# Kernel optimization log

Hardware: AMD Instinct MI355X
Metric: run time of the kernel (lower is better)

Reference implementation:

```python
import jax, jax.numpy as jnp
import numpy as np

B, D, N = 8, 512, 4096
HEADS, DH = 8, 64
HID = HEADS * DH  # 512
SCALE = DH ** -0.5


def setup_inputs() -> dict:
    key = jax.random.key(0)
    k0, k1, k2, k3 = jax.random.split(key, 4)
    x = jax.random.normal(k0, (B, D, N), dtype=jnp.float32)
    w_qkv = jax.random.normal(k1, (3 * HID, D), dtype=jnp.float32) * 0.02
    w_out = jax.random.normal(k2, (D, HID), dtype=jnp.float32) * 0.02
    b_out = jax.random.normal(k3, (D,), dtype=jnp.float32) * 0.02
    g = jnp.ones((1, D, 1), dtype=jnp.float32)
    return {"x": x, "w_qkv": w_qkv, "w_out": w_out, "b_out": b_out, "g": g}


def reference(x, w_qkv, w_out, b_out, g):
    # 1x1 Conv1d (no bias) == channel matmul: [b, 3*HID, n]
    qkv = jnp.einsum('od,bdn->bon', w_qkv, x)
    q, k, v = jnp.split(qkv, 3, axis=1)
    # b (h c) n -> b h c n
    q = q.reshape(B, HEADS, DH, N)
    k = k.reshape(B, HEADS, DH, N)
    v = v.reshape(B, HEADS, DH, N)
    q = jax.nn.softmax(q, axis=2) * SCALE  # softmax over feature dim d
    k = jax.nn.softmax(k, axis=3)          # softmax over sequence dim n
    context = jnp.einsum('bhdn,bhen->bhde', k, v)   # [b,h,d,e]
    out = jnp.einsum('bhde,bhdn->bhen', context, q)  # [b,h,e,n]
    out = out.reshape(B, HID, N)
    # 1x1 Conv1d with bias
    y = jnp.einsum('oh,bhn->bon', w_out, out) + b_out[None, :, None]
    # RMSNorm: F.normalize(y, dim=1) * g * sqrt(D)
    norm = jnp.sqrt(jnp.sum(y * y, axis=1, keepdims=True))
    y = y / jnp.maximum(norm, 1e-12) * g * jnp.asarray(D, y.dtype) ** 0.5
    return y
```

## Files before the change

### kernel.cpp

```cpp
#include <hip/hip_runtime.h>
#include <math.h>

#define B 8
#define D 512
#define N 4096
#define HEADS 8
#define DH 64
#define HID 512
#define O3 1536
#define KDIM 512
#define SCALE 0.125f
#define SQRT_D 22.62741699796952f

typedef __attribute__((ext_vector_type(4))) float f32x4;
typedef __attribute__((ext_vector_type(8))) short bf16x8;

static __device__ __forceinline__ unsigned short f2bf(float f) {
    unsigned int u = __float_as_uint(f);
    unsigned int r = (u + 0x7fffu + ((u >> 16) & 1u)) >> 16;
    return (unsigned short)r;
}

static __device__ __forceinline__ float bf2f(unsigned short u) {
    return __uint_as_float((unsigned int)u << 16);
}

static __device__ __forceinline__ void gload_lds16(const void* g, void* l) {
    __builtin_amdgcn_global_load_lds(
        (const __attribute__((address_space(1))) unsigned int*)g,
        (__attribute__((address_space(3))) unsigned int*)l, 16, 0, 0);
}

__global__ __launch_bounds__(256) void prep(const float* __restrict__ x,
                                            unsigned short* __restrict__ xT,
                                            const float* __restrict__ w,
                                            unsigned short* __restrict__ wb) {
    if (blockIdx.z == B) {
        int i = ((blockIdx.y * 96 + blockIdx.x) * 256 + threadIdx.x) * 4;
        float4 v = *(const float4*)(w + i);
        __align__(8) unsigned short o[4] = {f2bf(v.x), f2bf(v.y), f2bf(v.z), f2bf(v.w)};
        *(uint2*)(wb + i) = *(const uint2*)o;
        return;
    }
    if (blockIdx.x >= 64) return;
    __shared__ float tile[64][65];
    const int n0 = blockIdx.x * 64, d0 = blockIdx.y * 64, b = blockIdx.z;
    const float* xb = x + (size_t)b * D * N;
    unsigned short* xTb = xT + (size_t)b * N * KDIM;
    const int t = threadIdx.x;
    const int r = t >> 4, c4 = (t & 15) * 4;
#pragma unroll
    for (int i = 0; i < 4; ++i) {
        int row = r + i * 16;
        float4 v = *(const float4*)(xb + (size_t)(d0 + row) * N + n0 + c4);
        tile[row][c4 + 0] = v.x;
        tile[row][c4 + 1] = v.y;
        tile[row][c4 + 2] = v.z;
        tile[row][c4 + 3] = v.w;
    }
    __syncthreads();
#pragma unroll
    for (int pass = 0; pass < 2; ++pass) {
        int orow = (t >> 3) + pass * 32;
        int oc = (t & 7) * 8;
        __align__(16) unsigned short o[8];
#pragma unroll
        for (int e = 0; e < 8; ++e) o[e] = f2bf(tile[oc + e][orow]);
        *(uint4*)(xTb + (size_t)(n0 + orow) * KDIM + d0 + oc) = *(const uint4*)o;
    }
}

#define STAGE_H(PTR, REGION, TILE0, KT, H)                                         \
    _Pragma("unroll") for (int sub = 0; sub < 2; ++sub)                            \
        gload_lds16(PTR + (size_t)((TILE0) + (H) * 128 + spr[sub]) * KDIM          \
                        + (KT) * 64 + scoff[sub],                                  \
                    lds + (REGION) + ((KT) & 1) * 32768 + (H) * 16384              \
                        + sub * 8192 + t * 16);

#define PHASE_A(MG, KS)                                                            \
    _Pragma("unroll") for (int j = 0; j < 4; ++j)                                  \
        afr[j] = *(const bf16x8*)(lds + rbuf + arb + ((MG) * 4 + j) * 2048 + xa[KS]);

#define PHASE_B(KS)                                                               \
    _Pragma("unroll") for (int nf = 0; nf < 4; ++nf)                               \
        bfr[nf] = *(const bf16x8*)(lds + 65536 + rbuf + brb + nf * 2048 + xa[KS]);

#define PHASE_MMA(MG)                                                              \
    asm volatile("s_waitcnt lgkmcnt(0)" ::: "memory");                             \
    __builtin_amdgcn_sched_barrier(0);                                             \
    __builtin_amdgcn_s_setprio(1);                                                 \
    _Pragma("unroll") for (int j = 0; j < 4; ++j)                                  \
        _Pragma("unroll") for (int nf = 0; nf < 4; ++nf)                           \
            acc[(MG) * 4 + j][nf] = __builtin_amdgcn_mfma_f32_16x16x32_bf16(       \
                afr[j], bfr[nf], acc[(MG) * 4 + j][nf], 0, 0, 0);                  \
    __builtin_amdgcn_s_setprio(0);

#define GEMM256_CORE(A_PTR, BT_PTR)                                                \
    __shared__ __align__(16) char lds[131072];                                     \
    const int t = threadIdx.x;                                                     \
    const int lane = t & 63;                                                       \
    const int wid = t >> 6;                                                        \
    const int wm = wid >> 2, wn = wid & 3;                                         \
    int spr[2], scoff[2];                                                          \
    _Pragma("unroll") for (int sub = 0; sub < 2; ++sub) {                          \
        int p = sub * 8192 + t * 16;                                               \
        spr[sub] = p >> 7;                                                         \
        int spc = (p >> 4) & 7;                                                    \
        scoff[sub] = (spc ^ (spr[sub] & 7)) * 8;                                   \
    }                                                                              \
    int xa[2];                                                                     \
    _Pragma("unroll") for (int ks = 0; ks < 2; ++ks)                               \
        xa[ks] = ((ks * 4 + (lane >> 4)) ^ (lane & 7)) << 4;                       \
    const int arb = (wm * 128 + (lane & 15)) * 128;                                \
    const int brb = (wn * 64 + (lane & 15)) * 128;                                 \
    f32x4 acc[8][4] = {};                                                          \
    bf16x8 afr[4], bfr[4];                                                         \
    STAGE_H(A_PTR, 0, row0, 0, 0)                                                  \
    STAGE_H(A_PTR, 0, row0, 0, 1)                                                  \
    STAGE_H(BT_PTR, 65536, col0, 0, 0)                                             \
    STAGE_H(BT_PTR, 65536, col0, 0, 1)                                             \
    for (int kt = 0; kt < 8; ++kt) {                                               \
        const int rbuf = (kt & 1) * 32768;                                         \
        __builtin_amdgcn_s_barrier();                                              \
        if (kt < 7) {                                                              \
            STAGE_H(A_PTR, 0, row0, kt + 1, 0)                                     \
            STAGE_H(A_PTR, 0, row0, kt + 1, 1)                                     \
            STAGE_H(BT_PTR, 65536, col0, kt + 1, 0)                                \
            STAGE_H(BT_PTR, 65536, col0, kt + 1, 1)                                \
            asm volatile("s_waitcnt vmcnt(8)" ::: "memory");                       \
        } else {                                                                   \
            asm volatile("s_waitcnt vmcnt(0)" ::: "memory");                       \
        }                                                                          \
        __builtin_amdgcn_s_barrier();                                              \
        __builtin_amdgcn_sched_barrier(0);                                         \
        PHASE_A(0, 0) PHASE_B(0) PHASE_MMA(0)                                      \
        PHASE_A(1, 0) PHASE_MMA(1)                                                 \
        PHASE_A(0, 1) PHASE_B(1) PHASE_MMA(0)                                      \
        PHASE_A(1, 1) PHASE_MMA(1)                                                 \
    }

__global__ __launch_bounds__(512, 2) void gemm_qkv(const unsigned short* __restrict__ Aw,
                                                   const unsigned short* __restrict__ BTall,
                                                   unsigned short* __restrict__ qT,
                                                   unsigned short* __restrict__ kvall) {
    const int b = blockIdx.z;
    const unsigned short* A = Aw;
    const unsigned short* BT = BTall + (size_t)b * N * KDIM;
    const int row0 = blockIdx.y * 256;
    const int col0 = blockIdx.x * 256;
    GEMM256_CORE(A, BT)

    const int g = lane >> 4;
    if (blockIdx.y < 2) {
#pragma unroll
        for (int g2 = 0; g2 < 2; ++g2) {
            const int h = blockIdx.y * 4 + wm * 2 + g2;
#pragma unroll
            for (int nf = 0; nf < 4; ++nf) {
                float mx = -1e30f;
#pragma unroll
                for (int j = 0; j < 4; ++j)
#pragma unroll
                    for (int r = 0; r < 4; ++r) mx = fmaxf(mx, acc[g2 * 4 + j][nf][r]);
                mx = fmaxf(mx, __shfl_xor(mx, 16));
                mx = fmaxf(mx, __shfl_xor(mx, 32));
                float e[16];
                float s = 0.f;
#pragma unroll
                for (int j = 0; j < 4; ++j)
#pragma unroll
                    for (int r = 0; r < 4; ++r) {
                        e[j * 4 + r] = __expf(acc[g2 * 4 + j][nf][r] - mx);
                        s += e[j * 4 + r];
                    }
                s += __shfl_xor(s, 16);
                s += __shfl_xor(s, 32);
                float rs = SCALE / s;
                int n = col0 + wn * 64 + nf * 16 + (lane & 15);
                unsigned short* dst = qT + ((size_t)b * N + n) * KDIM + h * 64 + g * 4;
#pragma unroll
                for (int j = 0; j < 4; ++j) {
                    __align__(8) unsigned short o4[4] = {
                        f2bf(e[j * 4 + 0] * rs), f2bf(e[j * 4 + 1] * rs),
                        f2bf(e[j * 4 + 2] * rs), f2bf(e[j * 4 + 3] * rs)};
                    *(uint2*)(dst + j * 16) = *(const uint2*)o4;
                }
            }
        }
    } else {
        unsigned short* C = kvall + (size_t)b * 1024 * N;
        const int rbase = row0 - 512 + wm * 128;
#pragma unroll
        for (int mf = 0; mf < 8; ++mf) {
            int row_b = rbase + mf * 16 + g * 4;
#pragma unroll
            for (int nf = 0; nf < 4; ++nf) {
                int col = col0 + wn * 64 + nf * 16 + (lane & 15);
#pragma unroll
                for (int r = 0; r < 4; ++r)
                    C[(size_t)(row_b + r) * N + col] = f2bf(acc[mf][nf][r]);
            }
        }
    }
}

__global__ __launch_bounds__(256) void context_mfma3(const unsigned short* __restrict__ kvb,
                                                     float* __restrict__ ctx,
                                                     float* __restrict__ ksum) {
    const int ch = blockIdx.x, h = blockIdx.y, b = blockIdx.z;
    const int K0 = ch * 512;
    const unsigned short* kbase = kvb + ((size_t)b * 1024 + h * DH) * (size_t)N + K0;
    const unsigned short* vbase = kvb + ((size_t)b * 1024 + 512 + h * DH) * (size_t)N + K0;

    __shared__ __align__(16) unsigned short Ks[64 * 64];
    __shared__ __align__(16) unsigned short Vs[64 * 64];

    const int t = threadIdx.x;
    const int lane = t & 63;
    const int wv = t >> 6;

    const int kr = t >> 2;
    const int kc = (t & 3) * 16;
    const int kchunk0 = kc >> 3;
    const int kdst0 = kr * 128 + (((kchunk0 + 0) ^ (kr & 7)) << 4);
    const int kdst1 = kr * 128 + (((kchunk0 + 1) ^ (kr & 7)) << 4);

    int vrow[2], vcoff[2];
#pragma unroll
    for (int i = 0; i < 2; ++i) {
        int p = i * 4096 + t * 16;
        int pr = p >> 7;
        int pc = (p >> 4) & 7;
        vrow[i] = pr;
        vcoff[i] = (pc ^ (pr & 7)) * 8;
    }

    const int ar = wv * 16 + (lane & 15);
    int aoff[2], boff[4][2];
#pragma unroll
    for (int s = 0; s < 2; ++s) {
        int chunk = s * 4 + (lane >> 4);
        aoff[s] = ar * 128 + ((chunk ^ (ar & 7)) << 4);
#pragma unroll
        for (int nf = 0; nf < 4; ++nf) {
            int br = nf * 16 + (lane & 15);
            boff[nf][s] = br * 128 + ((chunk ^ (br & 7)) << 4);
        }
    }

    bf16x8 ones;
#pragma unroll
    for (int j = 0; j < 8; ++j) ones[j] = (short)0x3F80;

    f32x4 acc[4] = {};
    f32x4 accs = {};

    for (int k0 = 0; k0 < 512; k0 += 64) {
#pragma unroll
        for (int i = 0; i < 2; ++i)
            gload_lds16(vbase + (size_t)vrow[i] * N + k0 + vcoff[i],
                        (char*)Vs + i * 4096 + t * 16);
        __align__(16) unsigned short raw[16];
        *(uint4*)raw = *(const uint4*)(kbase + (size_t)kr * N + k0 + kc);
        *(uint4*)(raw + 8) = *(const uint4*)(kbase + (size_t)kr * N + k0 + kc + 8);
        __align__(16) unsigned short o[16];
#pragma unroll
        for (int j = 0; j < 16; ++j) o[j] = f2bf(__expf(bf2f(raw[j])));
        *(uint4*)((char*)Ks + kdst0) = *(const uint4*)o;
        *(uint4*)((char*)Ks + kdst1) = *(const uint4*)(o + 8);
        __syncthreads();

        bf16x8 av[2], bv[4][2];
#pragma unroll
        for (int s = 0; s < 2; ++s) {
            av[s] = *(const bf16x8*)((const char*)Ks + aoff[s]);
#pragma unroll
            for (int nf = 0; nf < 4; ++nf)
                bv[nf][s] = *(const bf16x8*)((const char*)Vs + boff[nf][s]);
        }
#pragma unroll
        for (int s = 0; s < 2; ++s) {
#pragma unroll
            for (int nf = 0; nf < 4; ++nf)
                acc[nf] = __builtin_amdgcn_mfma_f32_16x16x32_bf16(av[s], bv[nf][s], acc[nf], 0, 0, 0);
            accs = __builtin_amdgcn_mfma_f32_16x16x32_bf16(av[s], ones, accs, 0, 0, 0);
        }
        __syncthreads();
    }

    float* cbase = ctx + ((size_t)(b * HEADS + h)) * DH * DH;
    const int drow = wv * 16 + (lane >> 4) * 4;
#pragma unroll
    for (int nf = 0; nf < 4; ++nf) {
        int e = nf * 16 + (lane & 15);
#pragma unroll
        for (int rr = 0; rr < 4; ++rr)
            atomicAdd(&cbase[(drow + rr) * DH + e], acc[nf][rr]);
    }
    if ((lane & 15) == 0) {
#pragma unroll
        for (int rr = 0; rr < 4; ++rr)
            atomicAdd(&ksum[b * 512 + h * DH + drow + rr], accs[rr]);
    }
}

__global__ __launch_bounds__(256) void fold_wout3(const float* __restrict__ w_out,
                                                  const float* __restrict__ ctx,
                                                  const float* __restrict__ ksum,
                                                  unsigned short* __restrict__ w2) {
    const int ot = blockIdx.x, h = blockIdx.y, b = blockIdx.z;
    __shared__ __align__(16) unsigned short As[128 * 64];
    __shared__ __align__(16) unsigned short Bs[64 * 64];
    const int t = threadIdx.x;
    const int lane = t & 63;
    const int wv = t >> 6;

#pragma unroll
    for (int i = 0; i < 8; ++i) {
        int lin = t + i * 256;
        int r = lin >> 4;
        int c4 = (lin & 15) * 4;
        float4 v = *(const float4*)(w_out + (size_t)(ot * 128 + r) * HID + h * 64 + c4);
        __align__(8) unsigned short o4[4] = {f2bf(v.x), f2bf(v.y), f2bf(v.z), f2bf(v.w)};
        int chunk = c4 >> 3;
        int off = (c4 & 7) * 2;
        *(uint2*)((char*)As + r * 128 + ((chunk ^ (r & 7)) << 4) + off) = *(const uint2*)o4;
    }
    const float* cb = ctx + ((size_t)(b * HEADS + h)) * DH * DH;
    const float* ks = ksum + b * 512 + h * 64;
#pragma unroll
    for (int i = 0; i < 4; ++i) {
        int lin = t + i * 256;
        int r = lin >> 4;
        int c4 = (lin & 15) * 4;
        float inv = 1.0f / ks[r];
        float4 v = *(const float4*)(cb + (size_t)r * DH + c4);
        __align__(8) unsigned short o4[4] = {f2bf(v.x * inv), f2bf(v.y * inv),
                                             f2bf(v.z * inv), f2bf(v.w * inv)};
        int chunk = c4 >> 3;
        int off = (c4 & 7) * 2;
        *(uint2*)((char*)Bs + r * 128 + ((chunk ^ (r & 7)) << 4) + off) = *(const uint2*)o4;
    }
    __syncthreads();

    f32x4 acc[2][4] = {};
#pragma unroll
    for (int s = 0; s < 2; ++s) {
        int chunk = s * 4 + (lane >> 4);
        bf16x8 bf[4];
#pragma unroll
        for (int nf = 0; nf < 4; ++nf) {
            int brow = nf * 16 + (lane & 15);
            bf[nf] = *(const bf16x8*)((const char*)Bs + brow * 128 + ((chunk ^ (brow & 7)) << 4));
        }
#pragma unroll
        for (int mm = 0; mm < 2; ++mm) {
            int arow = (wv * 2 + mm) * 16 + (lane & 15);
            bf16x8 a = *(const bf16x8*)((const char*)As + arow * 128 + ((chunk ^ (arow & 7)) << 4));
#pragma unroll
            for (int nf = 0; nf < 4; ++nf)
                acc[mm][nf] = __builtin_amdgcn_mfma_f32_16x16x32_bf16(a, bf[nf], acc[mm][nf], 0, 0, 0);
        }
    }

#pragma unroll
    for (int mm = 0; mm < 2; ++mm) {
        int o_base = ot * 128 + (wv * 2 + mm) * 16 + (lane >> 4) * 4;
#pragma unroll
        for (int nf = 0; nf < 4; ++nf) {
            int d = nf * 16 + (lane & 15);
#pragma unroll
            for (int rr = 0; rr < 4; ++rr)
                w2[((size_t)(b * D) + o_base + rr) * D + h * 64 + d] = f2bf(acc[mm][nf][rr]);
        }
    }
}

#define YSTAGE(KT)                                                                 \
    _Pragma("unroll") for (int sub = 0; sub < 8; ++sub)                            \
        gload_lds16(A + (size_t)(sub * 64 + srow) * KDIM + (KT) * 64 + sco,        \
                    lds + ((KT) & 1) * 65536 + sub * 8192 + t * 16);               \
    gload_lds16(BT + (size_t)(col0 + srow) * KDIM + (KT) * 64 + sco,               \
                lds + 131072 + ((KT) & 1) * 8192 + t * 16);

__global__ __launch_bounds__(512, 1) void gemm_y_fused(const unsigned short* __restrict__ w2all,
                                                       const unsigned short* __restrict__ qTall,
                                                       const float* __restrict__ bias,
                                                       const float* __restrict__ g,
                                                       float* __restrict__ outall) {
    const int b = blockIdx.z;
    const unsigned short* A = w2all + (size_t)b * D * D;
    const unsigned short* BT = qTall + (size_t)b * N * KDIM;
    float* out = outall + (size_t)b * D * N;
    const int col0 = blockIdx.x * 64;

    __shared__ __align__(16) char lds[147456];
    const int t = threadIdx.x;
    const int lane = t & 63;
    const int wid = t >> 6;

    const int srow = t >> 3;
    const int sco = ((t & 7) ^ (srow & 7)) * 8;

    int xa[2];
#pragma unroll
    for (int ks = 0; ks < 2; ++ks)
        xa[ks] = ((ks * 4 + (lane >> 4)) ^ (lane & 7)) << 4;
    const int arb = (wid * 64 + (lane & 15)) * 128;
    const int brb = (lane & 15) * 128;

    f32x4 acc[4][4] = {};
    bf16x8 afr[4], bfr[4];

    YSTAGE(0)
    for (int kt = 0; kt < 8; ++kt) {
        const int abuf = (kt & 1) * 65536;
        const int bbuf = 131072 + (kt & 1) * 8192;
        __builtin_amdgcn_s_barrier();
        if (kt < 7) {
            YSTAGE(kt + 1)
            asm volatile("s_waitcnt vmcnt(9)" ::: "memory");
        } else {
            asm volatile("s_waitcnt vmcnt(0)" ::: "memory");
        }
        __builtin_amdgcn_s_barrier();
        __builtin_amdgcn_sched_barrier(0);
#pragma unroll
        for (int ks = 0; ks < 2; ++ks) {
#pragma unroll
            for (int mf = 0; mf < 4; ++mf)
                afr[mf] = *(const bf16x8*)(lds + abuf + arb + mf * 2048 + xa[ks]);
#pragma unroll
            for (int nf = 0; nf < 4; ++nf)
                bfr[nf] = *(const bf16x8*)(lds + bbuf + brb + nf * 2048 + xa[ks]);
            asm volatile("s_waitcnt lgkmcnt(0)" ::: "memory");
            __builtin_amdgcn_sched_barrier(0);
            __builtin_amdgcn_s_setprio(1);
#pragma unroll
            for (int mf = 0; mf < 4; ++mf)
#pragma unroll
                for (int nf = 0; nf < 4; ++nf)
                    acc[mf][nf] = __builtin_amdgcn_mfma_f32_16x16x32_bf16(
                        afr[mf], bfr[nf], acc[mf][nf], 0, 0, 0);
            __builtin_amdgcn_s_setprio(0);
        }
    }

    float csum[4] = {0.f, 0.f, 0.f, 0.f};
#pragma unroll
    for (int mf = 0; mf < 4; ++mf) {
        int row = wid * 64 + mf * 16 + (lane >> 4) * 4;
#pragma unroll
        for (int r = 0; r < 4; ++r) {
            float bv = bias[row + r];
#pragma unroll
            for (int nf = 0; nf < 4; ++nf) {
                acc[mf][nf][r] += bv;
                csum[nf] += acc[mf][nf][r] * acc[mf][nf][r];
            }
        }
    }
#pragma unroll
    for (int nf = 0; nf < 4; ++nf) {
        csum[nf] += __shfl_xor(csum[nf], 16);
        csum[nf] += __shfl_xor(csum[nf], 32);
    }
    __syncthreads();
    float* scr = (float*)lds;
    if (lane < 16) {
#pragma unroll
        for (int nf = 0; nf < 4; ++nf) scr[wid * 64 + nf * 16 + lane] = csum[nf];
    }
    __syncthreads();
    float rinv[4];
#pragma unroll
    for (int nf = 0; nf < 4; ++nf) {
        int c = nf * 16 + (lane & 15);
        float s = 0.f;
#pragma unroll
        for (int w = 0; w < 8; ++w) s += scr[w * 64 + c];
        rinv[nf] = SQRT_D / fmaxf(sqrtf(s), 1e-12f);
    }
#pragma unroll
    for (int mf = 0; mf < 4; ++mf) {
        int row = wid * 64 + mf * 16 + (lane >> 4) * 4;
#pragma unroll
        for (int r = 0; r < 4; ++r) {
            float gv = g[row + r];
#pragma unroll
            for (int nf = 0; nf < 4; ++nf) {
                int col = col0 + nf * 16 + (lane & 15);
                out[(size_t)(row + r) * N + col] = acc[mf][nf][r] * rinv[nf] * gv;
            }
        }
    }
}

extern "C" void kernel_launch(void* const* d_in, const int* in_sizes, int n_in,
                              void* d_out, int out_size, void* d_ws, size_t ws_size,
                              hipStream_t stream) {
    const float* x = (const float*)d_in[0];
    const float* w_qkv = (const float*)d_in[1];
    const float* w_out = (const float*)d_in[2];
    const float* b_out = (const float*)d_in[3];
    const float* g = (const float*)d_in[4];
    float* out = (float*)d_out;

    unsigned short* kvb = (unsigned short*)d_ws;
    float* ctx = (float*)(kvb + (size_t)B * 1024 * N);
    float* ksum = ctx + (size_t)B * HEADS * DH * DH;
    unsigned short* w2 = (unsigned short*)(ksum + B * 512);
    unsigned short* wqb = w2 + (size_t)B * D * D;
    unsigned short* xT = wqb + (size_t)O3 * KDIM;
    unsigned short* qT = xT + (size_t)B * N * KDIM;

    hipMemsetAsync(ctx, 0, ((size_t)B * HEADS * DH * DH + B * 512) * sizeof(float), stream);

    prep<<<dim3(96, 8, B + 1), 256, 0, stream>>>(x, xT, w_qkv, wqb);

    gemm_qkv<<<dim3(N / 256, O3 / 256, B), 512, 0, stream>>>(wqb, xT, qT, kvb);

    context_mfma3<<<dim3(8, HEADS, B), 256, 0, stream>>>(kvb, ctx, ksum);
    fold_wout3<<<dim3(4, HEADS, B), 256, 0, stream>>>(w_out, ctx, ksum, w2);

    gemm_y_fused<<<dim3(N / 64, 1, B), 512, 0, stream>>>(w2, qT, b_out, g, out);
}
```

Measured before the change: 145.8 us.

## Halve K-tile depth in QKV and output GEMMs to shrink LDS and raise occupancy

Both the QKV GEMM and the fused output GEMM now stage 32-wide K slices instead of 64-wide, doubling the number of K iterations. Shared memory per block drops by half, and launch bounds rise to allow four blocks per CU instead of one or two. The LDS swizzle and fragment addressing are redone for the narrower rows, and the y-kernel's B loads are restricted to half the threads, with wave-specific vmcnt waits. More resident blocks can hide latency, but the change adds twice as many barriers per tile and may cause register pressure under the tighter launch bounds.

```diff
diff --git a/kernel.cpp b/kernel.cpp
--- a/kernel.cpp
+++ b/kernel.cpp
@@ -70,22 +70,21 @@
     }
 }
 
-#define STAGE_H(PTR, REGION, TILE0, KT, H)                                         \
+#define STAGE32(PTR, REGION, TILE0, KT)                                            \
     _Pragma("unroll") for (int sub = 0; sub < 2; ++sub)                            \
-        gload_lds16(PTR + (size_t)((TILE0) + (H) * 128 + spr[sub]) * KDIM          \
-                        + (KT) * 64 + scoff[sub],                                  \
-                    lds + (REGION) + ((KT) & 1) * 32768 + (H) * 16384              \
-                        + sub * 8192 + t * 16);
-
-#define PHASE_A(MG, KS)                                                            \
+        gload_lds16(PTR + (size_t)((TILE0) + sub * 128 + (t >> 2)) * KDIM          \
+                        + (KT) * 32 + sco,                                         \
+                    lds + (REGION) + ((KT) & 1) * 16384 + sub * 8192 + t * 16);
+
+#define PHASE_A32(MG)                                                              \
     _Pragma("unroll") for (int j = 0; j < 4; ++j)                                  \
-        afr[j] = *(const bf16x8*)(lds + rbuf + arb + ((MG) * 4 + j) * 2048 + xa[KS]);
-
-#define PHASE_B(KS)                                                               \
+        afr[j] = *(const bf16x8*)(lds + rbuf + arb + ((MG) * 4 + j) * 1024 + xa);
+
+#define PHASE_B32                                                                  \
     _Pragma("unroll") for (int nf = 0; nf < 4; ++nf)                               \
-        bfr[nf] = *(const bf16x8*)(lds + 65536 + rbuf + brb + nf * 2048 + xa[KS]);
-
-#define PHASE_MMA(MG)                                                              \
+        bfr[nf] = *(const bf16x8*)(lds + 32768 + rbuf + brb + nf * 1024 + xa);
+
+#define PHASE_MMA32(MG)                                                            \
     asm volatile("s_waitcnt lgkmcnt(0)" ::: "memory");                             \
     __builtin_amdgcn_sched_barrier(0);                                             \
     __builtin_amdgcn_s_setprio(1);                                                 \
@@ -95,51 +94,37 @@
                 afr[j], bfr[nf], acc[(MG) * 4 + j][nf], 0, 0, 0);                  \
     __builtin_amdgcn_s_setprio(0);
 
-#define GEMM256_CORE(A_PTR, BT_PTR)                                                \
-    __shared__ __align__(16) char lds[131072];                                     \
+#define GEMM256_CORE32(A_PTR, BT_PTR)                                              \
+    __shared__ __align__(16) char lds[65536];                                      \
     const int t = threadIdx.x;                                                     \
     const int lane = t & 63;                                                       \
     const int wid = t >> 6;                                                        \
     const int wm = wid >> 2, wn = wid & 3;                                         \
-    int spr[2], scoff[2];                                                          \
-    _Pragma("unroll") for (int sub = 0; sub < 2; ++sub) {                          \
-        int p = sub * 8192 + t * 16;                                               \
-        spr[sub] = p >> 7;                                                         \
-        int spc = (p >> 4) & 7;                                                    \
-        scoff[sub] = (spc ^ (spr[sub] & 7)) * 8;                                   \
-    }                                                                              \
-    int xa[2];                                                                     \
-    _Pragma("unroll") for (int ks = 0; ks < 2; ++ks)                               \
-        xa[ks] = ((ks * 4 + (lane >> 4)) ^ (lane & 7)) << 4;                       \
-    const int arb = (wm * 128 + (lane & 15)) * 128;                                \
-    const int brb = (wn * 64 + (lane & 15)) * 128;                                 \
+    const int sco = ((t & 3) ^ ((t >> 3) & 3)) * 8;                                \
+    const int xa = (((lane >> 4) ^ (((lane & 15) >> 1) & 3))) << 4;                \
+    const int arb = (wm * 128 + (lane & 15)) * 64;                                 \
+    const int brb = (wn * 64 + (lane & 15)) * 64;                                  \
     f32x4 acc[8][4] = {};                                                          \
     bf16x8 afr[4], bfr[4];                                                         \
-    STAGE_H(A_PTR, 0, row0, 0, 0)                                                  \
-    STAGE_H(A_PTR, 0, row0, 0, 1)                                                  \
-    STAGE_H(BT_PTR, 65536, col0, 0, 0)                                             \
-    STAGE_H(BT_PTR, 65536, col0, 0, 1)                                             \
-    for (int kt = 0; kt < 8; ++kt) {                                               \
-        const int rbuf = (kt & 1) * 32768;                                         \
+    STAGE32(A_PTR, 0, row0, 0)                                                     \
+    STAGE32(BT_PTR, 32768, col0, 0)                                                \
+    for (int kt = 0; kt < 16; ++kt) {                                              \
+        const int rbuf = (kt & 1) * 16384;                                         \
         __builtin_amdgcn_s_barrier();                                              \
-        if (kt < 7) {                                                              \
-            STAGE_H(A_PTR, 0, row0, kt + 1, 0)                                     \
-            STAGE_H(A_PTR, 0, row0, kt + 1, 1)                                     \
-            STAGE_H(BT_PTR, 65536, col0, kt + 1, 0)                                \
-            STAGE_H(BT_PTR, 65536, col0, kt + 1, 1)                                \
-            asm volatile("s_waitcnt vmcnt(8)" ::: "memory");                       \
+        if (kt < 15) {                                                             \
+            STAGE32(A_PTR, 0, row0, kt + 1)                                        \
+            STAGE32(BT_PTR, 32768, col0, kt + 1)                                   \
+            asm volatile("s_waitcnt vmcnt(4)" ::: "memory");                       \
         } else {                                                                   \
             asm volatile("s_waitcnt vmcnt(0)" ::: "memory");                       \
         }                                                                          \
         __builtin_amdgcn_s_barrier();                                              \
         __builtin_amdgcn_sched_barrier(0);                                         \
-        PHASE_A(0, 0) PHASE_B(0) PHASE_MMA(0)                                      \
-        PHASE_A(1, 0) PHASE_MMA(1)                                                 \
-        PHASE_A(0, 1) PHASE_B(1) PHASE_MMA(0)                                      \
-        PHASE_A(1, 1) PHASE_MMA(1)                                                 \
-    }
-
-__global__ __launch_bounds__(512, 2) void gemm_qkv(const unsigned short* __restrict__ Aw,
+        PHASE_A32(0) PHASE_B32 PHASE_MMA32(0)                                      \
+        PHASE_A32(1) PHASE_MMA32(1)                                                \
+    }
+
+__global__ __launch_bounds__(512, 4) void gemm_qkv(const unsigned short* __restrict__ Aw,
                                                    const unsigned short* __restrict__ BTall,
                                                    unsigned short* __restrict__ qT,
                                                    unsigned short* __restrict__ kvall) {
@@ -148,7 +133,7 @@
     const unsigned short* BT = BTall + (size_t)b * N * KDIM;
     const int row0 = blockIdx.y * 256;
     const int col0 = blockIdx.x * 256;
-    GEMM256_CORE(A, BT)
+    GEMM256_CORE32(A, BT)
 
     const int g = lane >> 4;
     if (blockIdx.y < 2) {
@@ -376,14 +361,15 @@
     }
 }
 
-#define YSTAGE(KT)                                                                 \
-    _Pragma("unroll") for (int sub = 0; sub < 8; ++sub)                            \
-        gload_lds16(A + (size_t)(sub * 64 + srow) * KDIM + (KT) * 64 + sco,        \
-                    lds + ((KT) & 1) * 65536 + sub * 8192 + t * 16);               \
-    gload_lds16(BT + (size_t)(col0 + srow) * KDIM + (KT) * 64 + sco,               \
-                lds + 131072 + ((KT) & 1) * 8192 + t * 16);
-
-__global__ __launch_bounds__(512, 1) void gemm_y_fused(const unsigned short* __restrict__ w2all,
+#define YSTAGE32(KT)                                                               \
+    _Pragma("unroll") for (int sub = 0; sub < 4; ++sub)                            \
+        gload_lds16(A + (size_t)(sub * 128 + (t >> 2)) * KDIM + (KT) * 32 + sco,   \
+                    lds + ((KT) & 1) * 32768 + sub * 8192 + t * 16);               \
+    if (t < 256)                                                                   \
+        gload_lds16(BT + (size_t)(col0 + (t >> 2)) * KDIM + (KT) * 32 + sco,       \
+                    lds + 65536 + ((KT) & 1) * 4096 + t * 16);
+
+__global__ __launch_bounds__(512, 4) void gemm_y_fused(const unsigned short* __restrict__ w2all,
                                                        const unsigned short* __restrict__ qTall,
                                                        const float* __restrict__ bias,
                                                        const float* __restrict__ g,
@@ -394,56 +380,52 @@
     float* out = outall + (size_t)b * D * N;
     const int col0 = blockIdx.x * 64;
 
-    __shared__ __align__(16) char lds[147456];
+    __shared__ __align__(16) char lds[73728];
     const int t = threadIdx.x;
     const int lane = t & 63;
     const int wid = t >> 6;
 
-    const int srow = t >> 3;
-    const int sco = ((t & 7) ^ (srow & 7)) * 8;
-
-    int xa[2];
-#pragma unroll
-    for (int ks = 0; ks < 2; ++ks)
-        xa[ks] = ((ks * 4 + (lane >> 4)) ^ (lane & 7)) << 4;
-    const int arb = (wid * 64 + (lane & 15)) * 128;
-    const int brb = (lane & 15) * 128;
+    const int sco = ((t & 3) ^ ((t >> 3) & 3)) * 8;
+    const int xa = (((lane >> 4) ^ (((lane & 15) >> 1) & 3))) << 4;
+    const int arb = (wid * 64 + (lane & 15)) * 64;
+    const int brb = (lane & 15) * 64;
 
     f32x4 acc[4][4] = {};
     bf16x8 afr[4], bfr[4];
 
-    YSTAGE(0)
-    for (int kt = 0; kt < 8; ++kt) {
-        const int abuf = (kt & 1) * 65536;
-        const int bbuf = 131072 + (kt & 1) * 8192;
+    YSTAGE32(0)
+    for (int kt = 0; kt < 16; ++kt) {
+        const int abuf = (kt & 1) * 32768;
+        const int bbuf = 65536 + (kt & 1) * 4096;
         __builtin_amdgcn_s_barrier();
-        if (kt < 7) {
-            YSTAGE(kt + 1)
-            asm volatile("s_waitcnt vmcnt(9)" ::: "memory");
+        if (kt < 15) {
+            YSTAGE32(kt + 1)
+            if (wid < 4) {
+                asm volatile("s_waitcnt vmcnt(5)" ::: "memory");
+            } else {
+                asm volatile("s_waitcnt vmcnt(4)" ::: "memory");
+            }
         } else {
             asm volatile("s_waitcnt vmcnt(0)" ::: "memory");
         }
         __builtin_amdgcn_s_barrier();
         __builtin_amdgcn_sched_barrier(0);
 #pragma unroll
-        for (int ks = 0; ks < 2; ++ks) {
-#pragma unroll
-            for (int mf = 0; mf < 4; ++mf)
-                afr[mf] = *(const bf16x8*)(lds + abuf + arb + mf * 2048 + xa[ks]);
+        for (int mf = 0; mf < 4; ++mf)
+            afr[mf] = *(const bf16x8*)(lds + abuf + arb + mf * 1024 + xa);
+#pragma unroll
+        for (int nf = 0; nf < 4; ++nf)
+            bfr[nf] = *(const bf16x8*)(lds + bbuf + brb + nf * 1024 + xa);
+        asm volatile("s_waitcnt lgkmcnt(0)" ::: "memory");
+        __builtin_amdgcn_sched_barrier(0);
+        __builtin_amdgcn_s_setprio(1);
+#pragma unroll
+        for (int mf = 0; mf < 4; ++mf)
 #pragma unroll
             for (int nf = 0; nf < 4; ++nf)
-                bfr[nf] = *(const bf16x8*)(lds + bbuf + brb + nf * 2048 + xa[ks]);
-            asm volatile("s_waitcnt lgkmcnt(0)" ::: "memory");
-            __builtin_amdgcn_sched_barrier(0);
-            __builtin_amdgcn_s_setprio(1);
-#pragma unroll
-            for (int mf = 0; mf < 4; ++mf)
-#pragma unroll
-                for (int nf = 0; nf < 4; ++nf)
-                    acc[mf][nf] = __builtin_amdgcn_mfma_f32_16x16x32_bf16(
-                        afr[mf], bfr[nf], acc[mf][nf], 0, 0, 0);
-            __builtin_amdgcn_s_setprio(0);
-        }
+                acc[mf][nf] = __builtin_amdgcn_mfma_f32_16x16x32_bf16(
+                    afr[mf], bfr[nf], acc[mf][nf], 0, 0, 0);
+        __builtin_amdgcn_s_setprio(0);
     }
 
     float csum[4] = {0.f, 0.f, 0.f, 0.f};
```

Measured after the change: 493.2 us. 238% more time.

## Halve K-tile in output GEMM to cut LDS and allow two blocks per CU

Applied to the files above, without the earlier changes.

The fused output-projection GEMM now stages K in 32-wide tiles instead of 64, so the LDS footprint is halved and the launch bound no longer pins one block per CU. The staging, swizzle and fragment addressing are recomputed for the narrower tile, and the vmcnt waits are adjusted per wave because only half the threads load B. The aim is higher occupancy, letting a second block hide global-load latency. The cost is twice as many barriers and K iterations with less MFMA work between synchronizations.

```diff
diff --git a/kernel.cpp b/kernel.cpp
--- a/kernel.cpp
+++ b/kernel.cpp
@@ -376,74 +376,71 @@
     }
 }
 
-#define YSTAGE(KT)                                                                 \
-    _Pragma("unroll") for (int sub = 0; sub < 8; ++sub)                            \
-        gload_lds16(A + (size_t)(sub * 64 + srow) * KDIM + (KT) * 64 + sco,        \
-                    lds + ((KT) & 1) * 65536 + sub * 8192 + t * 16);               \
-    gload_lds16(BT + (size_t)(col0 + srow) * KDIM + (KT) * 64 + sco,               \
-                lds + 131072 + ((KT) & 1) * 8192 + t * 16);
-
-__global__ __launch_bounds__(512, 1) void gemm_y_fused(const unsigned short* __restrict__ w2all,
-                                                       const unsigned short* __restrict__ qTall,
-                                                       const float* __restrict__ bias,
-                                                       const float* __restrict__ g,
-                                                       float* __restrict__ outall) {
+#define YSTAGE32(KT)                                                               \
+    _Pragma("unroll") for (int sub = 0; sub < 4; ++sub)                            \
+        gload_lds16(A + (size_t)(sub * 128 + (t >> 2)) * KDIM + (KT) * 32 + sco,   \
+                    lds + ((KT) & 1) * 32768 + sub * 8192 + t * 16);               \
+    if (t < 256)                                                                   \
+        gload_lds16(BT + (size_t)(col0 + (t >> 2)) * KDIM + (KT) * 32 + sco,       \
+                    lds + 65536 + ((KT) & 1) * 4096 + t * 16);
+
+__global__ __launch_bounds__(512) void gemm_y_fused(const unsigned short* __restrict__ w2all,
+                                                    const unsigned short* __restrict__ qTall,
+                                                    const float* __restrict__ bias,
+                                                    const float* __restrict__ g,
+                                                    float* __restrict__ outall) {
     const int b = blockIdx.z;
     const unsigned short* A = w2all + (size_t)b * D * D;
     const unsigned short* BT = qTall + (size_t)b * N * KDIM;
     float* out = outall + (size_t)b * D * N;
     const int col0 = blockIdx.x * 64;
 
-    __shared__ __align__(16) char lds[147456];
+    __shared__ __align__(16) char lds[73728];
     const int t = threadIdx.x;
     const int lane = t & 63;
     const int wid = t >> 6;
 
-    const int srow = t >> 3;
-    const int sco = ((t & 7) ^ (srow & 7)) * 8;
-
-    int xa[2];
-#pragma unroll
-    for (int ks = 0; ks < 2; ++ks)
-        xa[ks] = ((ks * 4 + (lane >> 4)) ^ (lane & 7)) << 4;
-    const int arb = (wid * 64 + (lane & 15)) * 128;
-    const int brb = (lane & 15) * 128;
+    const int sco = ((t & 3) ^ ((t >> 3) & 3)) * 8;
+    const int xa = (((lane >> 4) ^ (((lane & 15) >> 1) & 3))) << 4;
+    const int arb = (wid * 64 + (lane & 15)) * 64;
+    const int brb = (lane & 15) * 64;
 
     f32x4 acc[4][4] = {};
     bf16x8 afr[4], bfr[4];
 
-    YSTAGE(0)
-    for (int kt = 0; kt < 8; ++kt) {
-        const int abuf = (kt & 1) * 65536;
-        const int bbuf = 131072 + (kt & 1) * 8192;
+    YSTAGE32(0)
+    for (int kt = 0; kt < 16; ++kt) {
+        const int abuf = (kt & 1) * 32768;
+        const int bbuf = 65536 + (kt & 1) * 4096;
         __builtin_amdgcn_s_barrier();
-        if (kt < 7) {
-            YSTAGE(kt + 1)
-            asm volatile("s_waitcnt vmcnt(9)" ::: "memory");
+        if (kt < 15) {
+            YSTAGE32(kt + 1)
+            if (wid < 4) {
+                asm volatile("s_waitcnt vmcnt(5)" ::: "memory");
+            } else {
+                asm volatile("s_waitcnt vmcnt(4)" ::: "memory");
+            }
         } else {
             asm volatile("s_waitcnt vmcnt(0)" ::: "memory");
         }
         __builtin_amdgcn_s_barrier();
         __builtin_amdgcn_sched_barrier(0);
 #pragma unroll
-        for (int ks = 0; ks < 2; ++ks) {
-#pragma unroll
-            for (int mf = 0; mf < 4; ++mf)
-                afr[mf] = *(const bf16x8*)(lds + abuf + arb + mf * 2048 + xa[ks]);
+        for (int mf = 0; mf < 4; ++mf)
+            afr[mf] = *(const bf16x8*)(lds + abuf + arb + mf * 1024 + xa);
+#pragma unroll
+        for (int nf = 0; nf < 4; ++nf)
+            bfr[nf] = *(const bf16x8*)(lds + bbuf + brb + nf * 1024 + xa);
+        asm volatile("s_waitcnt lgkmcnt(0)" ::: "memory");
+        __builtin_amdgcn_sched_barrier(0);
+        __builtin_amdgcn_s_setprio(1);
+#pragma unroll
+        for (int mf = 0; mf < 4; ++mf)
 #pragma unroll
             for (int nf = 0; nf < 4; ++nf)
-                bfr[nf] = *(const bf16x8*)(lds + bbuf + brb + nf * 2048 + xa[ks]);
-            asm volatile("s_waitcnt lgkmcnt(0)" ::: "memory");
-            __builtin_amdgcn_sched_barrier(0);
-            __builtin_amdgcn_s_setprio(1);
-#pragma unroll
-            for (int mf = 0; mf < 4; ++mf)
-#pragma unroll
-                for (int nf = 0; nf < 4; ++nf)
-                    acc[mf][nf] = __builtin_amdgcn_mfma_f32_16x16x32_bf16(
-                        afr[mf], bfr[nf], acc[mf][nf], 0, 0, 0);
-            __builtin_amdgcn_s_setprio(0);
-        }
+                acc[mf][nf] = __builtin_amdgcn_mfma_f32_16x16x32_bf16(
+                    afr[mf], bfr[nf], acc[mf][nf], 0, 0, 0);
+        __builtin_amdgcn_s_setprio(0);
     }
 
     float csum[4] = {0.f, 0.f, 0.f, 0.f};
```

Measured after the change: 149.4 us. 1.02x slower.
